# Performance work log

Hardware: AMD Instinct MI355X
Metric: run time of the kernel (lower is better)

The kernel has to match this reference:

```python
import jax, jax.numpy as jnp
import numpy as np

KERNEL_LEN = 512
INPUT_LEN = 65536


def setup_inputs() -> dict:
    key = jax.random.key(0)
    k1, k2 = jax.random.split(key)
    x = jax.random.normal(k1, (INPUT_LEN,), dtype=jnp.float32)
    kernel = jax.random.normal(k2, (KERNEL_LEN,), dtype=jnp.float32)
    return {"input": x, "kernel": kernel}


def _dtw_row(prev, d_row):
    # prev: accumulated_cost of previous row, shape [K]
    # ac[j] = min(prev[j-1], prev[j], ac[j-1]) + d[j]
    # Let c[j] = min(prev[j-1], prev[j]) + d[j]  (prev[-1] treated as +inf,
    # which reproduces ac[i,0] = prev[0] + d[0]).
    # Then ac[j] = min(c[j], ac[j-1] + d[j])
    #            = S[j] + cummin_k<=j (c[k] - S[k]),  S = inclusive cumsum of d.
    inf = jnp.full((1,), jnp.inf, dtype=d_row.dtype)
    prev_shift = jnp.concatenate([inf, prev[:-1]])
    c = jnp.minimum(prev_shift, prev) + d_row
    S = jnp.cumsum(d_row)
    ac = S + jax.lax.cummin(c - S)
    return ac, ac[-1]


def reference(input, kernel):
    # pairwise squared distances: [input_len, kernel_len]
    d = (kernel[None, :] - input[:, None]) ** 2
    # row 0: cumulative sum along kernel axis
    prev0 = jnp.cumsum(d[0])
    # rows 1..N-1 via scan with wavefront-free min-plus row update
    _, lasts = jax.lax.scan(_dtw_row, prev0, d[1:])
    # return accumulated_cost[:, kernel_len - 1]
    return jnp.concatenate([prev0[-1:], lasts])
```

## Files before the change

kernel.cpp:

```cpp
#include <hip/hip_runtime.h>


#define K_LEN 512
#define N_LEN 65536
#define PAD_L 512
#define PAD_R 1024
#define XPAD_TOTAL (PAD_L + N_LEN + PAD_R)
#define BIGX 1e20f
#define NCHUNK 1032
#define RING 256

__global__ void dtw_pad_kernel(const float* __restrict__ x, float* __restrict__ xpad) {
    int i = blockIdx.x * blockDim.x + threadIdx.x;
    if (i < XPAD_TOTAL) {
        int j = i - PAD_L;
        xpad[i] = (j >= 0 && j < N_LEN) ? x[j] : BIGX;
    }
}

template <bool LAST>
__device__ __forceinline__ void dtw_chunk(int c, const float* __restrict__ xl,
                                          const float* __restrict__ ldsIn,
                                          float* __restrict__ ldsOut,
                                          float k0, float k1,
                                          float& A0, float& A1, float& E0, float& E1,
                                          float& xp, int lane, float* __restrict__ out) {
    const int t0 = c * 64;
    const int rb = (c & 3) * 64;

    float xv[64];
#pragma unroll
    for (int r = 0; r < 64; ++r) xv[r] = xl[t0 + r];

    float binv[64];
    binv[0] = ldsIn[(rb + RING - 1) & (RING - 1)];
#pragma unroll
    for (int r = 1; r < 64; ++r) binv[r] = ldsIn[rb + r - 1];

    float keep[64];

#pragma unroll
    for (int r = 0; r < 64; ++r) {
        const float xf = xv[r];
        const float esh0 = __int_as_float(__builtin_amdgcn_update_dpp(
            __float_as_int(binv[r]), __float_as_int(E1), 0x138 , 0xF, 0xF, false));
        const float esh1 = E0;
        float d0 = k0 - xf; d0 *= d0;
        float d1 = k1 - xp; d1 *= d1;
        const float na0 = fminf(A0, esh0) + d0;
        const float na1 = fminf(A1, esh1) + d1;
        const float ne0 = fminf(na0, A0);
        const float ne1 = fminf(na1, A1);
        keep[r] = LAST ? na1 : ne1;
        A0 = na0; A1 = na1; E0 = ne0; E1 = ne1; xp = xf;
    }

    if (lane == 63) {
#pragma unroll
        for (int r = 0; r < 64; ++r) ldsOut[rb + r] = keep[r];
    }

    if (LAST) {
        const float ov = ldsOut[rb + lane];
        const int oi = t0 + lane - (K_LEN - 1);
        if (oi >= 0 && oi < N_LEN) out[oi] = ov;
    }
}

__global__ __launch_bounds__(256, 1) void dtw_main(const float* __restrict__ xpad,
                                                   const float* __restrict__ kern,
                                                   float* __restrict__ out) {
    __shared__ float lds[5 * RING];
    const float INFV = __builtin_inff();
    const int tid  = threadIdx.x;
    const int w    = __builtin_amdgcn_readfirstlane(tid) >> 6;
    const int lane = tid & 63;

    for (int i = tid; i < 5 * RING; i += 256)
        lds[i] = (i == 4 * RING + RING - 1) ? 0.0f : INFV;
    __syncthreads();

    const int j0 = w * 128 + 2 * lane;
    const float k0 = kern[j0];
    const float k1 = kern[j0 + 1];

    const float* xl = xpad + (PAD_L - j0);
    float xp = xl[-1];

    float* ldsOut      = lds + w * RING;
    const float* ldsIn = (w == 0) ? (lds + 4 * RING) : (lds + (w - 1) * RING);

    float A0 = INFV, A1 = INFV, E0 = INFV, E1 = INFV;

    for (int S = 0; S < NCHUNK + 3; ++S) {
        const int c = S - w;
        if (c >= 0 && c < NCHUNK) {
            if (w == 3)
                dtw_chunk<true>(c, xl, ldsIn, ldsOut, k0, k1, A0, A1, E0, E1, xp, lane, out);
            else
                dtw_chunk<false>(c, xl, ldsIn, ldsOut, k0, k1, A0, A1, E0, E1, xp, lane, out);
        }
        if (S == 0 && tid == 0) lds[4 * RING + RING - 1] = INFV;
        __syncthreads();
    }
}

extern "C" void kernel_launch(void* const* d_in, const int* in_sizes, int n_in,
                              void* d_out, int out_size, void* d_ws, size_t ws_size,
                              hipStream_t stream) {
    const float* x = (const float*)d_in[0];
    const float* k = (const float*)d_in[1];
    float* xpad = (float*)d_ws;
    float* out  = (float*)d_out;
    dtw_pad_kernel<<<(XPAD_TOTAL + 255) / 256, 256, 0, stream>>>(x, xpad);
    dtw_main<<<1, 256, 0, stream>>>(xpad, k, out);
}
```

Before: 2.132 ms.

## Keep DTW boundary values in registers via DPP shifts and double-buffer input loads

Replaces the per-chunk 64-entry register arrays for boundary inputs and kept outputs with single per-lane registers that rotate across the wave using DPP row shifts. Every lane now writes its own LDS slot instead of lane 63 writing all 64 values serially. It also drops the E0 state in favour of tracking the previous A0, loads x as float2 in two alternating 8-element buffers, and uses fma for the distance update. The plain __syncthreads is replaced by an inline waitcnt plus s_barrier, and the ring shrinks to 4 slots. The intent is to cut register pressure, serialized LDS stores and the instructions on the critical recurrence path, at the cost of extra DPP ops per step and a hand-written barrier whose memory ordering is less clearly guaranteed.

```diff
diff --git a/kernel.cpp b/kernel.cpp
--- a/kernel.cpp
+++ b/kernel.cpp
@@ -10,6 +10,8 @@
 #define NCHUNK 1032
 #define RING 256
 
+typedef float f32x2 __attribute__((ext_vector_type(2)));
+
 __global__ void dtw_pad_kernel(const float* __restrict__ x, float* __restrict__ xpad) {
     int i = blockIdx.x * blockDim.x + threadIdx.x;
     if (i < XPAD_TOTAL) {
@@ -18,66 +20,81 @@
     }
 }
 
+__device__ __forceinline__ float dpp_wave_shr1(float oldv, float src) {
+    return __int_as_float(__builtin_amdgcn_update_dpp(
+        __float_as_int(oldv), __float_as_int(src), 0x138, 0xF, 0xF, false));
+}
+__device__ __forceinline__ float dpp_wave_shl1(float oldv, float src) {
+    return __int_as_float(__builtin_amdgcn_update_dpp(
+        __float_as_int(oldv), __float_as_int(src), 0x130, 0xF, 0xF, false));
+}
+
 template <bool LAST>
 __device__ __forceinline__ void dtw_chunk(int c, const float* __restrict__ xl,
                                           const float* __restrict__ ldsIn,
                                           float* __restrict__ ldsOut,
                                           float k0, float k1,
-                                          float& A0, float& A1, float& E0, float& E1,
+                                          float& A0, float& A0p, float& A1, float& E1,
                                           float& xp, int lane, float* __restrict__ out) {
     const int t0 = c * 64;
     const int rb = (c & 3) * 64;
 
-    float xv[64];
+    float binvreg = ldsIn[(rb + lane - 1) & (RING - 1)];
+    float keepreg = 0.0f;
+
+    const f32x2* __restrict__ xl2 = (const f32x2*)(xl + t0);
+
+    auto ITER = [&](float xf) {
+        const float esh0 = dpp_wave_shr1(binvreg, E1);
+        binvreg = dpp_wave_shl1(binvreg, binvreg);
+        const float t0v = k0 - xf;
+        const float na0 = __builtin_fmaf(t0v, t0v, fminf(A0, esh0));
+        const float t1v = k1 - xp;
+        const float m1  = fminf(A0p, fminf(A1, A0));
+        const float na1 = __builtin_fmaf(t1v, t1v, m1);
+        const float ne1 = fminf(na1, A1);
+        keepreg = dpp_wave_shl1(LAST ? na1 : ne1, keepreg);
+        A0p = A0; A0 = na0; A1 = na1; E1 = ne1; xp = xf;
+    };
+
+    auto LOAD8 = [&](f32x2 (&X)[8], int base) {
 #pragma unroll
-    for (int r = 0; r < 64; ++r) xv[r] = xl[t0 + r];
+        for (int q = 0; q < 8; ++q) X[q] = xl2[base + q];
+    };
+    auto BLOCK16 = [&](const f32x2 (&X)[8]) {
+#pragma unroll
+        for (int q = 0; q < 8; ++q) { ITER(X[q].x); ITER(X[q].y); }
+    };
 
-    float binv[64];
-    binv[0] = ldsIn[(rb + RING - 1) & (RING - 1)];
-#pragma unroll
-    for (int r = 1; r < 64; ++r) binv[r] = ldsIn[rb + r - 1];
+    f32x2 xA[8], xB[8];
+    LOAD8(xA, 0);
+    LOAD8(xB, 8);
+    BLOCK16(xA);
+    LOAD8(xA, 16);
+    BLOCK16(xB);
+    LOAD8(xB, 24);
+    BLOCK16(xA);
+    BLOCK16(xB);
 
-    float keep[64];
-
-#pragma unroll
-    for (int r = 0; r < 64; ++r) {
-        const float xf = xv[r];
-        const float esh0 = __int_as_float(__builtin_amdgcn_update_dpp(
-            __float_as_int(binv[r]), __float_as_int(E1), 0x138 , 0xF, 0xF, false));
-        const float esh1 = E0;
-        float d0 = k0 - xf; d0 *= d0;
-        float d1 = k1 - xp; d1 *= d1;
-        const float na0 = fminf(A0, esh0) + d0;
-        const float na1 = fminf(A1, esh1) + d1;
-        const float ne0 = fminf(na0, A0);
-        const float ne1 = fminf(na1, A1);
-        keep[r] = LAST ? na1 : ne1;
-        A0 = na0; A1 = na1; E0 = ne0; E1 = ne1; xp = xf;
-    }
-
-    if (lane == 63) {
-#pragma unroll
-        for (int r = 0; r < 64; ++r) ldsOut[rb + r] = keep[r];
-    }
-
-    if (LAST) {
-        const float ov = ldsOut[rb + lane];
+    if (!LAST) {
+        ldsOut[rb + lane] = keepreg;
+    } else {
         const int oi = t0 + lane - (K_LEN - 1);
-        if (oi >= 0 && oi < N_LEN) out[oi] = ov;
+        if (oi >= 0 && oi < N_LEN) out[oi] = keepreg;
     }
 }
 
 __global__ __launch_bounds__(256, 1) void dtw_main(const float* __restrict__ xpad,
                                                    const float* __restrict__ kern,
                                                    float* __restrict__ out) {
-    __shared__ float lds[5 * RING];
+    __shared__ float lds[4 * RING];
     const float INFV = __builtin_inff();
     const int tid  = threadIdx.x;
     const int w    = __builtin_amdgcn_readfirstlane(tid) >> 6;
     const int lane = tid & 63;
 
-    for (int i = tid; i < 5 * RING; i += 256)
-        lds[i] = (i == 4 * RING + RING - 1) ? 0.0f : INFV;
+    for (int i = tid; i < 4 * RING; i += 256)
+        lds[i] = (i == 4 * RING - 1) ? 0.0f : INFV;
     __syncthreads();
 
     const int j0 = w * 128 + 2 * lane;
@@ -88,20 +105,20 @@
     float xp = xl[-1];
 
     float* ldsOut      = lds + w * RING;
-    const float* ldsIn = (w == 0) ? (lds + 4 * RING) : (lds + (w - 1) * RING);
+    const float* ldsIn = (w == 0) ? (lds + 3 * RING) : (lds + (w - 1) * RING);
 
-    float A0 = INFV, A1 = INFV, E0 = INFV, E1 = INFV;
+    float A0 = INFV, A0p = INFV, A1 = INFV, E1 = INFV;
 
     for (int S = 0; S < NCHUNK + 3; ++S) {
         const int c = S - w;
         if (c >= 0 && c < NCHUNK) {
             if (w == 3)
-                dtw_chunk<true>(c, xl, ldsIn, ldsOut, k0, k1, A0, A1, E0, E1, xp, lane, out);
+                dtw_chunk<true>(c, xl, ldsIn, ldsOut, k0, k1, A0, A0p, A1, E1, xp, lane, out);
             else
-                dtw_chunk<false>(c, xl, ldsIn, ldsOut, k0, k1, A0, A1, E0, E1, xp, lane, out);
+                dtw_chunk<false>(c, xl, ldsIn, ldsOut, k0, k1, A0, A0p, A1, E1, xp, lane, out);
         }
-        if (S == 0 && tid == 0) lds[4 * RING + RING - 1] = INFV;
-        __syncthreads();
+        if (S == 0 && tid == 0) lds[4 * RING - 1] = INFV;
+        asm volatile("s_waitcnt lgkmcnt(0)\n\ts_barrier" ::: "memory");
     }
 }
 
```

Measured after the change: 2.242 ms. 5.2% more time.
